# Optimization experiments

Measured on AMD Instinct MI355X. Metric: run time of the kernel, lower is better.

Reference implementation:

```python
import jax, jax.numpy as jnp
import numpy as np

MAX_DEG = 10   # max_degree in DuvenaudMPNN
T = 4          # num_timesteps
NUM_GRAPHS = 64


def setup_inputs() -> dict:
    key = jax.random.key(0)
    ks = jax.random.split(key, 10)
    N, E, IN, EC = 20000, 160000, 64, 16
    s = 0.1
    x = jax.random.normal(ks[0], (N, IN), dtype=jnp.float32)
    edge_index = jax.random.randint(ks[1], (2, E), 0, N)
    edge_attr = jax.random.normal(ks[2], (E, EC), dtype=jnp.float32)
    batch = jnp.sort(jax.random.randint(ks[3], (N,), 0, NUM_GRAPHS))
    # per-timestep, per-degree expert Linear(in+e -> in, bias=False)
    W_msg = jax.random.normal(ks[4], (T, MAX_DEG, IN + EC, IN), dtype=jnp.float32) * s
    # per-timestep readout Linear(in -> 10, bias=False)
    W_read = jax.random.normal(ks[5], (T, IN, 10), dtype=jnp.float32) * s
    fc1_w = jax.random.normal(ks[6], (10, 128), dtype=jnp.float32) * s
    fc1_b = jnp.zeros((128,), jnp.float32)
    fc2_w = jax.random.normal(ks[7], (128, 64), dtype=jnp.float32) * s
    fc2_b = jnp.zeros((64,), jnp.float32)
    fc3_w = jax.random.normal(ks[8], (64, 1), dtype=jnp.float32) * s
    fc3_b = jnp.zeros((1,), jnp.float32)
    return {"x": x, "edge_attr": edge_attr, "W_msg": W_msg, "W_read": W_read,
            "fc1_w": fc1_w, "fc1_b": fc1_b, "fc2_w": fc2_w, "fc2_b": fc2_b,
            "fc3_w": fc3_w, "fc3_b": fc3_b, "edge_index": edge_index, "batch": batch}


def _mpnn(x, edge_attr, W_msg, W_read, edge_index):
    N = x.shape[0]
    # add_self_loops: append (i,i) edges with zero edge features
    self_idx = jnp.arange(N, dtype=edge_index.dtype)
    src = jnp.concatenate([edge_index[0], self_idx])
    dst = jnp.concatenate([edge_index[1], self_idx])
    ea = jnp.concatenate([edge_attr, jnp.zeros((N, edge_attr.shape[1]), edge_attr.dtype)], axis=0)
    # degree of source node (incl. self loop), clamped to MAX_DEG; bucket 0..MAX_DEG-1
    deg = jax.ops.segment_sum(jnp.ones_like(src), src, num_segments=N)
    bucket = jnp.minimum(deg[src], MAX_DEG) - 1
    Etot = src.shape[0]
    for t in range(T):
        mi = jnp.concatenate([x[src], ea], axis=-1)           # [Etot, IN+EC]
        msgs = jnp.zeros((Etot, x.shape[1]), x.dtype)
        for d in range(MAX_DEG):                               # degree-bucketed experts
            md = jax.nn.sigmoid(mi @ W_msg[t, d])              # [Etot, IN]
            msgs = jnp.where((bucket == d)[:, None], md, msgs)
        x = jax.ops.segment_sum(msgs, dst, num_segments=N)    # aggr='add'
    # readout: all timestep heads applied to final x, softmax over outputs, summed
    node_out = jax.nn.softmax(x @ W_read[0], axis=1)
    for t in range(1, T):
        node_out = node_out + jax.nn.softmax(x @ W_read[t], axis=1)
    return node_out                                            # [N, 10]


def reference(x, edge_attr, W_msg, W_read, fc1_w, fc1_b, fc2_w, fc2_b, fc3_w, fc3_b, edge_index, batch):
    node_out = _mpnn(x, edge_attr, W_msg, W_read, edge_index)
    pooled = jax.ops.segment_sum(node_out, batch, num_segments=NUM_GRAPHS)  # global_add_pool
    h = jax.nn.leaky_relu(pooled @ fc1_w + fc1_b)
    h = jax.nn.leaky_relu(h @ fc2_w + fc2_b)
    return jax.nn.leaky_relu(h @ fc3_w + fc3_b)                # [NUM_GRAPHS, 1]
```

## Files before the change

kernel.cpp:

```cpp
#include <hip/hip_runtime.h>

#define MAXD 10
#define TSTEPS 4
#define KD 80
#define IN 64
#define ECH 16
#define TILE_N 64
#define SCAN_CHUNK 1024

#define AGG_BLOCK 512
#define GEPW 8
#define AGG_EPB (AGG_BLOCK / 16 * GEPW)

__device__ __forceinline__ float sigmoidf(float v) {
    return 1.0f / (1.0f + __expf(-v));
}


__global__ __launch_bounds__(256) void hist_kernel(const int* __restrict__ ei,
                                                   int* deg, int* in_cnt, int E) {
    int e = blockIdx.x * 256 + threadIdx.x;
    if (e < E) {
        atomicAdd(&deg[ei[e]], 1);
        atomicAdd(&in_cnt[ei[E + e]], 1);
    }
}


__global__ __launch_bounds__(256) void scanA_kernel(const int* __restrict__ in_cnt,
                                                    const int* __restrict__ deg,
                                                    int* bsum, int* nb_cnt, int N) {
    __shared__ int part[256];
    __shared__ int nbh[MAXD];
    const int t = threadIdx.x;
    if (t < MAXD) nbh[t] = 0;
    __syncthreads();
    const int base = blockIdx.x * SCAN_CHUNK + t * 4;
    int s = 0;
    #pragma unroll
    for (int i = 0; i < 4; ++i) {
        int gi = base + i;
        if (gi < N) {
            s += in_cnt[gi];
            int dg = deg[gi];
            int b = (dg < MAXD - 1) ? dg : (MAXD - 1);
            atomicAdd(&nbh[b], 1);
        }
    }
    part[t] = s;
    __syncthreads();
    for (int off = 128; off > 0; off >>= 1) {
        if (t < off) part[t] += part[t + off];
        __syncthreads();
    }
    if (t == 0) bsum[blockIdx.x] = part[0];
    if (t < MAXD && nbh[t] > 0) atomicAdd(&nb_cnt[t], nbh[t]);
}

__global__ __launch_bounds__(256) void scanB_kernel(int* bsum, int nb,
                                                    const int* __restrict__ nb_cnt,
                                                    int* nb_cursor) {
    __shared__ int part[256];
    const int t = threadIdx.x;
    int v = (t < nb) ? bsum[t] : 0;
    part[t] = v;
    __syncthreads();
    for (int off = 1; off < 256; off <<= 1) {
        int add = (t >= off) ? part[t - off] : 0;
        __syncthreads();
        part[t] += add;
        __syncthreads();
    }
    if (t < nb) bsum[t] = part[t] - v;
    if (t == 0) {
        int acc = 0;
        for (int b = 0; b < MAXD; ++b) { nb_cursor[b] = acc; acc += nb_cnt[b]; }
    }
}

__global__ __launch_bounds__(256) void scanC_kernel(const int* __restrict__ in_cnt,
                                                    const int* __restrict__ bsum,
                                                    int* cursorN, int N) {
    __shared__ int part[256];
    const int t = threadIdx.x;
    const int base = blockIdx.x * SCAN_CHUNK + t * 4;
    int v[4] = {0, 0, 0, 0};
    #pragma unroll
    for (int i = 0; i < 4; ++i) if (base + i < N) v[i] = in_cnt[base + i];
    const int s = v[0] + v[1] + v[2] + v[3];
    part[t] = s;
    __syncthreads();
    for (int off = 1; off < 256; off <<= 1) {
        int add = (t >= off) ? part[t - off] : 0;
        __syncthreads();
        part[t] += add;
        __syncthreads();
    }
    int a = bsum[blockIdx.x] + part[t] - s;
    #pragma unroll
    for (int i = 0; i < 4; ++i) {
        if (base + i < N) cursorN[base + i] = a;
        a += v[i];
    }
}

__global__ __launch_bounds__(256) void nb_scatter_kernel(const int* __restrict__ deg,
                                                         int* cursor, int* node_list, int N) {
    __shared__ int h[MAXD];
    __shared__ int base[MAXD];
    const int t = threadIdx.x;
    if (t < MAXD) h[t] = 0;
    __syncthreads();
    const int n = blockIdx.x * 256 + t;
    int b = 0, loc = 0;
    const bool valid = n < N;
    if (valid) {
        int dg = deg[n];
        b = (dg < MAXD - 1) ? dg : (MAXD - 1);
        loc = atomicAdd(&h[b], 1);
    }
    __syncthreads();
    if (t < MAXD) base[t] = (h[t] > 0) ? atomicAdd(&cursor[t], h[t]) : 0;
    __syncthreads();
    if (valid) node_list[base[b] + loc] = n;
}

__global__ __launch_bounds__(256) void csr_scatter_kernel(
    const int* __restrict__ ei, const float* __restrict__ ea, const int* __restrict__ deg,
    int* cursor, int* src_csr, int* dst_csr, int* bkt_csr, float* ea_csr, int E)
{
    int e = blockIdx.x * 256 + threadIdx.x;
    if (e >= E) return;
    int s = ei[e], d = ei[E + e];
    int dg = deg[s];
    int b = (dg < MAXD - 1) ? dg : (MAXD - 1);
    int pos = atomicAdd(&cursor[d], 1);
    src_csr[pos] = s;
    dst_csr[pos] = d;
    bkt_csr[pos] = b;
    const float4* p = (const float4*)(ea + (size_t)e * ECH);
    float4* o = (float4*)(ea_csr + (size_t)pos * ECH);
    o[0] = p[0]; o[1] = p[1]; o[2] = p[2]; o[3] = p[3];
}


__global__ __launch_bounds__(256) void y_kernel(
    const float* __restrict__ xin, float* __restrict__ y, float* __restrict__ out,
    const int* __restrict__ node_list, const int* __restrict__ deg,
    const float* __restrict__ Wt, int N)
{
    __shared__ float Ws[IN][IN];
    __shared__ float Ms[IN][TILE_N + 4];
    __shared__ int id_s[TILE_N];
    __shared__ int bkt_s[TILE_N];

    const int t = threadIdx.x;
    const int i0 = blockIdx.x * TILE_N;
    const int ntile = min(TILE_N, N - i0);

    {
        const int e = t >> 2;
        const bool valid = e < ntile;
        const int c0 = (t & 3) * 16;
        const float4 z4 = make_float4(0.f, 0.f, 0.f, 0.f);
        int node = valid ? node_list[i0 + e] : 0;
        const float* xp = xin + (size_t)node * IN + c0;
        #pragma unroll
        for (int i = 0; i < 16; i += 4) {
            float4 v = valid ? *(const float4*)(xp + i) : z4;
            Ms[c0 + i + 0][e] = v.x; Ms[c0 + i + 1][e] = v.y;
            Ms[c0 + i + 2][e] = v.z; Ms[c0 + i + 3][e] = v.w;
        }
        if (t < TILE_N) {
            if (t < ntile) {
                int id = node_list[i0 + t];
                id_s[t] = id;
                int dg = deg[id];
                bkt_s[t] = (dg < MAXD - 1) ? dg : (MAXD - 1);
            } else { id_s[t] = 0; bkt_s[t] = -1; }
        }
    }
    __syncthreads();

    const int b_first = bkt_s[0];
    const int b_last = bkt_s[ntile - 1];
    const int eg4 = (t >> 4) * 4;
    const int cg4 = (t & 15) * 4;

    for (int b = b_first; b <= b_last; ++b) {
        if (b != b_first) __syncthreads();
        {
            const float4* Wb = (const float4*)(Wt + (size_t)b * KD * IN);
            float4* Wsp = (float4*)Ws;
            #pragma unroll
            for (int q = 0; q < 4; ++q) Wsp[t + q * 256] = Wb[t + q * 256];
        }
        __syncthreads();

        float acc[4][4];
        #pragma unroll
        for (int e2 = 0; e2 < 4; ++e2)
            #pragma unroll
            for (int c = 0; c < 4; ++c) acc[e2][c] = 0.f;

        #pragma unroll 8
        for (int k = 0; k < IN; ++k) {
            const float4 w = *(const float4*)&Ws[k][cg4];
            const float4 m = *(const float4*)&Ms[k][eg4];
            const float me[4] = {m.x, m.y, m.z, m.w};
            #pragma unroll
            for (int e2 = 0; e2 < 4; ++e2) {
                acc[e2][0] += me[e2] * w.x;
                acc[e2][1] += me[e2] * w.y;
                acc[e2][2] += me[e2] * w.z;
                acc[e2][3] += me[e2] * w.w;
            }
        }

        #pragma unroll
        for (int e2 = 0; e2 < 4; ++e2) {
            const int el = eg4 + e2;
            if (el < ntile && bkt_s[el] == b) {
                const size_t o = (size_t)id_s[el] * IN + cg4;
                float4 v = make_float4(acc[e2][0], acc[e2][1], acc[e2][2], acc[e2][3]);
                *(float4*)(y + o) = v;
                float4 sv = make_float4(sigmoidf(v.x), sigmoidf(v.y),
                                        sigmoidf(v.z), sigmoidf(v.w));
                *(float4*)(out + o) = sv;
            }
        }
    }
}


__global__ __launch_bounds__(AGG_BLOCK) void agg5_kernel(
    const float* __restrict__ y, float* __restrict__ out,
    const int* __restrict__ src_csr, const int* __restrict__ dst_csr,
    const int* __restrict__ bkt_csr, const float* __restrict__ ea_csr,
    const float* __restrict__ Wt, int E)
{
    __shared__ float WeL[MAXD][ECH][IN];
    const int t = threadIdx.x;
    {
        const float4* Wsrc = (const float4*)Wt;
        float4* Wd = (float4*)WeL;
        #pragma unroll
        for (int i = 0; i < MAXD * ECH * IN / 4 / AGG_BLOCK; ++i) {
            int q = t + i * AGG_BLOCK;
            int b = q >> 8;
            int r = q & 255;
            Wd[q] = Wsrc[b * (KD * IN / 4) + (IN * IN / 4) + r];
        }
    }
    __syncthreads();

    const int lane = t & 63;
    const int grp = lane >> 4;
    const int gl = lane & 15;
    const int c0 = gl * 4;
    const int base = blockIdx.x * AGG_EPB + (t >> 6) * (4 * GEPW) + grp * GEPW;
    const int cnt = min(GEPW, E - base);
    if (cnt <= 0) return;

    const int m_idx = base + (gl & (GEPW - 1));
    int s_r = 0, d_r = -1, b_r = 0;
    if (m_idx < E) { s_r = src_csr[m_idx]; d_r = dst_csr[m_idx]; b_r = bkt_csr[m_idx]; }
    const int lane0 = grp * 16;

    float4 yv[GEPW];
    #pragma unroll
    for (int i = 0; i < GEPW; ++i) {
        int si = __shfl(s_r, lane0 + i);
        if (i < cnt) yv[i] = *(const float4*)(y + (size_t)si * IN + c0);
    }

    const float4* eab = (const float4*)(ea_csr + (size_t)base * ECH);
    float4 ca0, ca1, ca2, ca3;
    ca0 = eab[0]; ca1 = eab[1]; ca2 = eab[2]; ca3 = eab[3];

    int cur_d = __shfl(d_r, lane0);
    float4 acc = make_float4(0.f, 0.f, 0.f, 0.f);

    #pragma unroll
    for (int i = 0; i < GEPW; ++i) {
        if (i < cnt) {
            float4 na0, na1, na2, na3;
            if (i + 1 < cnt) {
                const float4* ep = (const float4*)(ea_csr + (size_t)(base + i + 1) * ECH);
                na0 = ep[0]; na1 = ep[1]; na2 = ep[2]; na3 = ep[3];
            } else {
                na0 = na1 = na2 = na3 = make_float4(0.f, 0.f, 0.f, 0.f);
            }
            const int b = __shfl(b_r, lane0 + i);
            const int d = __shfl(d_r, lane0 + i);
            if (d != cur_d) {
                float* op = out + (size_t)cur_d * IN + c0;
                atomicAdd(op + 0, acc.x); atomicAdd(op + 1, acc.y);
                atomicAdd(op + 2, acc.z); atomicAdd(op + 3, acc.w);
                acc = make_float4(0.f, 0.f, 0.f, 0.f);
                cur_d = d;
            }
            const float ev[16] = {ca0.x, ca0.y, ca0.z, ca0.w, ca1.x, ca1.y, ca1.z, ca1.w,
                                  ca2.x, ca2.y, ca2.z, ca2.w, ca3.x, ca3.y, ca3.z, ca3.w};
            float4 z = make_float4(0.f, 0.f, 0.f, 0.f);
            #pragma unroll
            for (int k = 0; k < ECH; ++k) {
                const float4 w = *(const float4*)&WeL[b][k][c0];
                z.x += ev[k] * w.x; z.y += ev[k] * w.y;
                z.z += ev[k] * w.z; z.w += ev[k] * w.w;
            }
            acc.x += sigmoidf(yv[i].x + z.x);
            acc.y += sigmoidf(yv[i].y + z.y);
            acc.z += sigmoidf(yv[i].z + z.z);
            acc.w += sigmoidf(yv[i].w + z.w);
            ca0 = na0; ca1 = na1; ca2 = na2; ca3 = na3;
        }
    }
    float* op = out + (size_t)cur_d * IN + c0;
    atomicAdd(op + 0, acc.x); atomicAdd(op + 1, acc.y);
    atomicAdd(op + 2, acc.z); atomicAdd(op + 3, acc.w);
}


__global__ __launch_bounds__(256) void readout_kernel(
    const float* __restrict__ x, const float* __restrict__ Wr,
    const int* __restrict__ batch, float* __restrict__ pooled, int N)
{
    __shared__ float Wr_s[TSTEPS][10][IN];
    __shared__ float pool_s[64 * 10];
    const int t = threadIdx.x;
    for (int idx = t; idx < TSTEPS * IN * 10; idx += 256) {
        int tt = idx / (IN * 10);
        int r = idx % (IN * 10);
        int k = r / 10;
        int j = r % 10;
        Wr_s[tt][j][k] = Wr[idx];
    }
    for (int idx = t; idx < 64 * 10; idx += 256) pool_s[idx] = 0.f;
    __syncthreads();

    const int n = blockIdx.x * 256 + t;
    if (n < N) {
        float xr[IN];
        const float4* xp = (const float4*)(x + (size_t)n * IN);
        #pragma unroll
        for (int i = 0; i < IN / 4; ++i) ((float4*)xr)[i] = xp[i];
        float out10[10];
        #pragma unroll
        for (int j = 0; j < 10; ++j) out10[j] = 0.f;
        for (int tt = 0; tt < TSTEPS; ++tt) {
            float lg[10];
            #pragma unroll
            for (int j = 0; j < 10; ++j) {
                const float4* wp = (const float4*)Wr_s[tt][j];
                float s = 0.f;
                #pragma unroll
                for (int i = 0; i < IN / 4; ++i) {
                    float4 w = wp[i];
                    float4 xv = ((const float4*)xr)[i];
                    s += w.x * xv.x + w.y * xv.y + w.z * xv.z + w.w * xv.w;
                }
                lg[j] = s;
            }
            float mx = lg[0];
            #pragma unroll
            for (int j = 1; j < 10; ++j) mx = fmaxf(mx, lg[j]);
            float sum = 0.f;
            #pragma unroll
            for (int j = 0; j < 10; ++j) { lg[j] = __expf(lg[j] - mx); sum += lg[j]; }
            float inv = 1.f / sum;
            #pragma unroll
            for (int j = 0; j < 10; ++j) out10[j] += lg[j] * inv;
        }
        const int g = batch[n];
        #pragma unroll
        for (int j = 0; j < 10; ++j) atomicAdd(&pool_s[g * 10 + j], out10[j]);
    }
    __syncthreads();
    for (int idx = t; idx < 64 * 10; idx += 256) {
        float v = pool_s[idx];
        if (v != 0.f) atomicAdd(&pooled[idx], v);
    }
}


__global__ __launch_bounds__(256) void mlp_kernel(
    const float* __restrict__ pooled,
    const float* __restrict__ fc1w, const float* __restrict__ fc1b,
    const float* __restrict__ fc2w, const float* __restrict__ fc2b,
    const float* __restrict__ fc3w, const float* __restrict__ fc3b,
    float* __restrict__ out, int G)
{
    __shared__ float p_s[64 * 10];
    __shared__ float h1[64 * 128];
    __shared__ float h2[64 * 64];
    const int t = threadIdx.x;
    for (int idx = t; idx < G * 10; idx += 256) p_s[idx] = pooled[idx];
    __syncthreads();
    for (int idx = t; idx < G * 128; idx += 256) {
        int g = idx >> 7, j = idx & 127;
        float s = fc1b[j];
        #pragma unroll
        for (int k = 0; k < 10; ++k) s += p_s[g * 10 + k] * fc1w[k * 128 + j];
        h1[idx] = (s > 0.f) ? s : 0.01f * s;
    }
    __syncthreads();
    for (int idx = t; idx < G * 64; idx += 256) {
        int g = idx >> 6, j = idx & 63;
        float s = fc2b[j];
        for (int k = 0; k < 128; ++k) s += h1[(g << 7) + k] * fc2w[(k << 6) + j];
        h2[idx] = (s > 0.f) ? s : 0.01f * s;
    }
    __syncthreads();
    if (t < G) {
        float s = fc3b[0];
        for (int k = 0; k < 64; ++k) s += h2[(t << 6) + k] * fc3w[k];
        out[t] = (s > 0.f) ? s : 0.01f * s;
    }
}


extern "C" void kernel_launch(void* const* d_in, const int* in_sizes, int n_in,
                              void* d_out, int out_size, void* d_ws, size_t ws_size,
                              hipStream_t stream)
{
    const float* x     = (const float*)d_in[0];
    const float* ea    = (const float*)d_in[1];
    const float* Wmsg  = (const float*)d_in[2];
    const float* Wread = (const float*)d_in[3];
    const float* fc1w  = (const float*)d_in[4];
    const float* fc1b  = (const float*)d_in[5];
    const float* fc2w  = (const float*)d_in[6];
    const float* fc2b  = (const float*)d_in[7];
    const float* fc3w  = (const float*)d_in[8];
    const float* fc3b  = (const float*)d_in[9];
    const int* ei      = (const int*)d_in[10];
    const int* batch   = (const int*)d_in[11];

    const int N = in_sizes[0] / IN;
    const int E = in_sizes[10] / 2;
    const int nscan = (N + SCAN_CHUNK - 1) / SCAN_CHUNK;

    char* ws = (char*)d_ws;
    size_t off = 0;
    auto take = [&](size_t bytes) {
        char* p = ws + off;
        off = (off + bytes + 255) & ~(size_t)255;
        return p;
    };
    int* meta      = (int*)take(128);
    float* pooled  = (float*)take(64 * 10 * 4);
    int* deg       = (int*)take((size_t)N * 4);
    int* in_cnt    = (int*)take((size_t)N * 4);
    const size_t zero_bytes = (size_t)((char*)in_cnt - (char*)meta) + (size_t)N * 4;
    int* bsum      = (int*)take((size_t)nscan * 4);
    int* node_list = (int*)take((size_t)N * 4);
    int* cursorN   = (int*)take((size_t)N * 4);
    int* src_csr   = (int*)take((size_t)E * 4);
    int* dst_csr   = (int*)take((size_t)E * 4);
    int* bkt_csr   = (int*)take((size_t)E * 4);
    float* ea_csr  = (float*)take((size_t)E * ECH * 4);
    float* ybuf    = (float*)take((size_t)N * IN * 4);
    float* xbA     = (float*)take((size_t)N * IN * 4);
    float* xbB     = (float*)take((size_t)N * IN * 4);

    int* nb_cnt    = meta;
    int* nb_cursor = meta + 16;

    const int nbN = (N + 255) / 256;
    const int nbE = (E + 255) / 256;

    hipMemsetAsync(meta, 0, zero_bytes, stream);
    hist_kernel<<<nbE, 256, 0, stream>>>(ei, deg, in_cnt, E);
    scanA_kernel<<<nscan, 256, 0, stream>>>(in_cnt, deg, bsum, nb_cnt, N);
    scanB_kernel<<<1, 256, 0, stream>>>(bsum, nscan, nb_cnt, nb_cursor);
    scanC_kernel<<<nscan, 256, 0, stream>>>(in_cnt, bsum, cursorN, N);
    nb_scatter_kernel<<<nbN, 256, 0, stream>>>(deg, nb_cursor, node_list, N);
    csr_scatter_kernel<<<nbE, 256, 0, stream>>>(ei, ea, deg, cursorN,
                                                src_csr, dst_csr, bkt_csr, ea_csr, E);

    const int nblkY = (N + TILE_N - 1) / TILE_N;
    const int nblkA = (E + AGG_EPB - 1) / AGG_EPB;
    const float* xi = x;
    float* bufs[2] = {xbA, xbB};
    for (int tt = 0; tt < TSTEPS; ++tt) {
        const float* Wt = Wmsg + (size_t)tt * MAXD * KD * IN;
        float* xo = bufs[tt & 1];
        y_kernel<<<nblkY, 256, 0, stream>>>(xi, ybuf, xo, node_list, deg, Wt, N);
        agg5_kernel<<<nblkA, AGG_BLOCK, 0, stream>>>(ybuf, xo, src_csr, dst_csr,
                                                     bkt_csr, ea_csr, Wt, E);
        xi = xo;
    }

    readout_kernel<<<nbN, 256, 0, stream>>>(xi, Wread, batch, pooled, N);
    mlp_kernel<<<1, 256, 0, stream>>>(pooled, fc1w, fc1b, fc2w, fc2b, fc3w, fc3b,
                                      (float*)d_out, out_size);
}
```

Baseline: 337.9 us.

## Switch edge aggregation to destination-owned CSR rows, removing atomics

The aggregation kernel now assigns one 16-lane group per destination node and walks that node's CSR row through a new row_ptr array, in place of fixed 8-edge chunks that flush partial sums with float atomics. The self-loop sigmoid term moves from y_kernel into the aggregation, which writes each output row once with a plain store. This drops the dst_csr array, the per-edge destination shuffles and the global atomics. The cost is load imbalance across nodes with different in-degrees, and the wave occupancy now depends on N instead of E.

New measurement: 322.0 us. 1.05x faster.

```diff
diff --git a/kernel.cpp b/kernel.cpp
--- a/kernel.cpp
+++ b/kernel.cpp
@@ -7,10 +7,6 @@
 #define ECH 16
 #define TILE_N 64
 #define SCAN_CHUNK 1024
-
-#define AGG_BLOCK 512
-#define GEPW 8
-#define AGG_EPB (AGG_BLOCK / 16 * GEPW)
 
 __device__ __forceinline__ float sigmoidf(float v) {
     return 1.0f / (1.0f + __expf(-v));
@@ -59,7 +55,8 @@
 
 __global__ __launch_bounds__(256) void scanB_kernel(int* bsum, int nb,
                                                     const int* __restrict__ nb_cnt,
-                                                    int* nb_cursor) {
+                                                    int* nb_cursor, int* row_ptr,
+                                                    int N, int E) {
     __shared__ int part[256];
     const int t = threadIdx.x;
     int v = (t < nb) ? bsum[t] : 0;
@@ -75,12 +72,13 @@
     if (t == 0) {
         int acc = 0;
         for (int b = 0; b < MAXD; ++b) { nb_cursor[b] = acc; acc += nb_cnt[b]; }
+        row_ptr[N] = E;
     }
 }
 
 __global__ __launch_bounds__(256) void scanC_kernel(const int* __restrict__ in_cnt,
                                                     const int* __restrict__ bsum,
-                                                    int* cursorN, int N) {
+                                                    int* cursorN, int* row_ptr, int N) {
     __shared__ int part[256];
     const int t = threadIdx.x;
     const int base = blockIdx.x * SCAN_CHUNK + t * 4;
@@ -99,7 +97,7 @@
     int a = bsum[blockIdx.x] + part[t] - s;
     #pragma unroll
     for (int i = 0; i < 4; ++i) {
-        if (base + i < N) cursorN[base + i] = a;
+        if (base + i < N) { cursorN[base + i] = a; row_ptr[base + i] = a; }
         a += v[i];
     }
 }
@@ -127,7 +125,7 @@
 
 __global__ __launch_bounds__(256) void csr_scatter_kernel(
     const int* __restrict__ ei, const float* __restrict__ ea, const int* __restrict__ deg,
-    int* cursor, int* src_csr, int* dst_csr, int* bkt_csr, float* ea_csr, int E)
+    int* cursor, int* src_csr, int* bkt_csr, float* ea_csr, int E)
 {
     int e = blockIdx.x * 256 + threadIdx.x;
     if (e >= E) return;
@@ -136,7 +134,6 @@
     int b = (dg < MAXD - 1) ? dg : (MAXD - 1);
     int pos = atomicAdd(&cursor[d], 1);
     src_csr[pos] = s;
-    dst_csr[pos] = d;
     bkt_csr[pos] = b;
     const float4* p = (const float4*)(ea + (size_t)e * ECH);
     float4* o = (float4*)(ea_csr + (size_t)pos * ECH);
@@ -145,7 +142,7 @@
 
 
 __global__ __launch_bounds__(256) void y_kernel(
-    const float* __restrict__ xin, float* __restrict__ y, float* __restrict__ out,
+    const float* __restrict__ xin, float* __restrict__ y,
     const int* __restrict__ node_list, const int* __restrict__ deg,
     const float* __restrict__ Wt, int N)
 {
@@ -222,22 +219,19 @@
             const int el = eg4 + e2;
             if (el < ntile && bkt_s[el] == b) {
                 const size_t o = (size_t)id_s[el] * IN + cg4;
-                float4 v = make_float4(acc[e2][0], acc[e2][1], acc[e2][2], acc[e2][3]);
-                *(float4*)(y + o) = v;
-                float4 sv = make_float4(sigmoidf(v.x), sigmoidf(v.y),
-                                        sigmoidf(v.z), sigmoidf(v.w));
-                *(float4*)(out + o) = sv;
+                *(float4*)(y + o) = make_float4(acc[e2][0], acc[e2][1],
+                                                acc[e2][2], acc[e2][3]);
             }
         }
     }
 }
 
 
-__global__ __launch_bounds__(AGG_BLOCK) void agg5_kernel(
+__global__ __launch_bounds__(512) void agg6_kernel(
     const float* __restrict__ y, float* __restrict__ out,
-    const int* __restrict__ src_csr, const int* __restrict__ dst_csr,
+    const int* __restrict__ row_ptr, const int* __restrict__ src_csr,
     const int* __restrict__ bkt_csr, const float* __restrict__ ea_csr,
-    const float* __restrict__ Wt, int E)
+    const float* __restrict__ Wt, int N)
 {
     __shared__ float WeL[MAXD][ECH][IN];
     const int t = threadIdx.x;
@@ -245,8 +239,8 @@
         const float4* Wsrc = (const float4*)Wt;
         float4* Wd = (float4*)WeL;
         #pragma unroll
-        for (int i = 0; i < MAXD * ECH * IN / 4 / AGG_BLOCK; ++i) {
-            int q = t + i * AGG_BLOCK;
+        for (int i = 0; i < MAXD * ECH * IN / 4 / 512; ++i) {
+            int q = t + i * 512;
             int b = q >> 8;
             int r = q & 255;
             Wd[q] = Wsrc[b * (KD * IN / 4) + (IN * IN / 4) + r];
@@ -258,67 +252,64 @@
     const int grp = lane >> 4;
     const int gl = lane & 15;
     const int c0 = gl * 4;
-    const int base = blockIdx.x * AGG_EPB + (t >> 6) * (4 * GEPW) + grp * GEPW;
-    const int cnt = min(GEPW, E - base);
-    if (cnt <= 0) return;
-
-    const int m_idx = base + (gl & (GEPW - 1));
-    int s_r = 0, d_r = -1, b_r = 0;
-    if (m_idx < E) { s_r = src_csr[m_idx]; d_r = dst_csr[m_idx]; b_r = bkt_csr[m_idx]; }
+    const int d = blockIdx.x * 32 + (t >> 6) * 4 + grp;
+    if (d >= N) return;
     const int lane0 = grp * 16;
 
-    float4 yv[GEPW];
-    #pragma unroll
-    for (int i = 0; i < GEPW; ++i) {
-        int si = __shfl(s_r, lane0 + i);
-        if (i < cnt) yv[i] = *(const float4*)(y + (size_t)si * IN + c0);
-    }
-
-    const float4* eab = (const float4*)(ea_csr + (size_t)base * ECH);
-    float4 ca0, ca1, ca2, ca3;
-    ca0 = eab[0]; ca1 = eab[1]; ca2 = eab[2]; ca3 = eab[3];
-
-    int cur_d = __shfl(d_r, lane0);
+    const int p0 = row_ptr[d];
+    const int p1 = row_ptr[d + 1];
+
     float4 acc = make_float4(0.f, 0.f, 0.f, 0.f);
 
-    #pragma unroll
-    for (int i = 0; i < GEPW; ++i) {
-        if (i < cnt) {
-            float4 na0, na1, na2, na3;
-            if (i + 1 < cnt) {
-                const float4* ep = (const float4*)(ea_csr + (size_t)(base + i + 1) * ECH);
-                na0 = ep[0]; na1 = ep[1]; na2 = ep[2]; na3 = ep[3];
-            } else {
-                na0 = na1 = na2 = na3 = make_float4(0.f, 0.f, 0.f, 0.f);
+    for (int p = p0; p < p1; p += 8) {
+        const int cnt = min(8, p1 - p);
+        const int mi = p + (gl & 7);
+        int s_r = 0, b_r = 0;
+        if (mi < p1) { s_r = src_csr[mi]; b_r = bkt_csr[mi]; }
+
+        float4 yv[8];
+        #pragma unroll
+        for (int i = 0; i < 8; ++i) {
+            int si = __shfl(s_r, lane0 + i);
+            if (i < cnt) yv[i] = *(const float4*)(y + (size_t)si * IN + c0);
+        }
+
+        const float4* eab = (const float4*)(ea_csr + (size_t)p * ECH);
+        float4 ca0 = eab[0], ca1 = eab[1], ca2 = eab[2], ca3 = eab[3];
+
+        #pragma unroll
+        for (int i = 0; i < 8; ++i) {
+            if (i < cnt) {
+                float4 na0, na1, na2, na3;
+                if (i + 1 < cnt) {
+                    const float4* ep = (const float4*)(ea_csr + (size_t)(p + i + 1) * ECH);
+                    na0 = ep[0]; na1 = ep[1]; na2 = ep[2]; na3 = ep[3];
+                } else {
+                    na0 = na1 = na2 = na3 = make_float4(0.f, 0.f, 0.f, 0.f);
+                }
+                const int b = __shfl(b_r, lane0 + i);
+                const float ev[16] = {ca0.x, ca0.y, ca0.z, ca0.w, ca1.x, ca1.y, ca1.z, ca1.w,
+                                      ca2.x, ca2.y, ca2.z, ca2.w, ca3.x, ca3.y, ca3.z, ca3.w};
+                float4 z = make_float4(0.f, 0.f, 0.f, 0.f);
+                #pragma unroll
+                for (int k = 0; k < ECH; ++k) {
+                    const float4 w = *(const float4*)&WeL[b][k][c0];
+                    z.x += ev[k] * w.x; z.y += ev[k] * w.y;
+                    z.z += ev[k] * w.z; z.w += ev[k] * w.w;
+                }
+                acc.x += sigmoidf(yv[i].x + z.x);
+                acc.y += sigmoidf(yv[i].y + z.y);
+                acc.z += sigmoidf(yv[i].z + z.z);
+                acc.w += sigmoidf(yv[i].w + z.w);
+                ca0 = na0; ca1 = na1; ca2 = na2; ca3 = na3;
             }
-            const int b = __shfl(b_r, lane0 + i);
-            const int d = __shfl(d_r, lane0 + i);
-            if (d != cur_d) {
-                float* op = out + (size_t)cur_d * IN + c0;
-                atomicAdd(op + 0, acc.x); atomicAdd(op + 1, acc.y);
-                atomicAdd(op + 2, acc.z); atomicAdd(op + 3, acc.w);
-                acc = make_float4(0.f, 0.f, 0.f, 0.f);
-                cur_d = d;
-            }
-            const float ev[16] = {ca0.x, ca0.y, ca0.z, ca0.w, ca1.x, ca1.y, ca1.z, ca1.w,
-                                  ca2.x, ca2.y, ca2.z, ca2.w, ca3.x, ca3.y, ca3.z, ca3.w};
-            float4 z = make_float4(0.f, 0.f, 0.f, 0.f);
-            #pragma unroll
-            for (int k = 0; k < ECH; ++k) {
-                const float4 w = *(const float4*)&WeL[b][k][c0];
-                z.x += ev[k] * w.x; z.y += ev[k] * w.y;
-                z.z += ev[k] * w.z; z.w += ev[k] * w.w;
-            }
-            acc.x += sigmoidf(yv[i].x + z.x);
-            acc.y += sigmoidf(yv[i].y + z.y);
-            acc.z += sigmoidf(yv[i].z + z.z);
-            acc.w += sigmoidf(yv[i].w + z.w);
-            ca0 = na0; ca1 = na1; ca2 = na2; ca3 = na3;
-        }
-    }
-    float* op = out + (size_t)cur_d * IN + c0;
-    atomicAdd(op + 0, acc.x); atomicAdd(op + 1, acc.y);
-    atomicAdd(op + 2, acc.z); atomicAdd(op + 3, acc.w);
+        }
+    }
+
+    const float4 yd = *(const float4*)(y + (size_t)d * IN + c0);
+    float4 r = make_float4(sigmoidf(yd.x) + acc.x, sigmoidf(yd.y) + acc.y,
+                           sigmoidf(yd.z) + acc.z, sigmoidf(yd.w) + acc.w);
+    *(float4*)(out + (size_t)d * IN + c0) = r;
 }
 
 
@@ -456,8 +447,8 @@
     int* bsum      = (int*)take((size_t)nscan * 4);
     int* node_list = (int*)take((size_t)N * 4);
     int* cursorN   = (int*)take((size_t)N * 4);
+    int* row_ptr   = (int*)take((size_t)(N + 1) * 4);
     int* src_csr   = (int*)take((size_t)E * 4);
-    int* dst_csr   = (int*)take((size_t)E * 4);
     int* bkt_csr   = (int*)take((size_t)E * 4);
     float* ea_csr  = (float*)take((size_t)E * ECH * 4);
     float* ybuf    = (float*)take((size_t)N * IN * 4);
@@ -473,22 +464,22 @@
     hipMemsetAsync(meta, 0, zero_bytes, stream);
     hist_kernel<<<nbE, 256, 0, stream>>>(ei, deg, in_cnt, E);
     scanA_kernel<<<nscan, 256, 0, stream>>>(in_cnt, deg, bsum, nb_cnt, N);
-    scanB_kernel<<<1, 256, 0, stream>>>(bsum, nscan, nb_cnt, nb_cursor);
-    scanC_kernel<<<nscan, 256, 0, stream>>>(in_cnt, bsum, cursorN, N);
+    scanB_kernel<<<1, 256, 0, stream>>>(bsum, nscan, nb_cnt, nb_cursor, row_ptr, N, E);
+    scanC_kernel<<<nscan, 256, 0, stream>>>(in_cnt, bsum, cursorN, row_ptr, N);
     nb_scatter_kernel<<<nbN, 256, 0, stream>>>(deg, nb_cursor, node_list, N);
     csr_scatter_kernel<<<nbE, 256, 0, stream>>>(ei, ea, deg, cursorN,
-                                                src_csr, dst_csr, bkt_csr, ea_csr, E);
+                                                src_csr, bkt_csr, ea_csr, E);
 
     const int nblkY = (N + TILE_N - 1) / TILE_N;
-    const int nblkA = (E + AGG_EPB - 1) / AGG_EPB;
+    const int nblkA = (N + 31) / 32;
     const float* xi = x;
     float* bufs[2] = {xbA, xbB};
     for (int tt = 0; tt < TSTEPS; ++tt) {
         const float* Wt = Wmsg + (size_t)tt * MAXD * KD * IN;
         float* xo = bufs[tt & 1];
-        y_kernel<<<nblkY, 256, 0, stream>>>(xi, ybuf, xo, node_list, deg, Wt, N);
-        agg5_kernel<<<nblkA, AGG_BLOCK, 0, stream>>>(ybuf, xo, src_csr, dst_csr,
-                                                     bkt_csr, ea_csr, Wt, E);
+        y_kernel<<<nblkY, 256, 0, stream>>>(xi, ybuf, node_list, deg, Wt, N);
+        agg6_kernel<<<nblkA, 512, 0, stream>>>(ybuf, xo, row_ptr, src_csr,
+                                               bkt_csr, ea_csr, Wt, N);
         xi = xo;
     }
 
```
